# Optimization experiments

Measured on AMD Instinct MI355X. Metric: run time of the kernel, lower is better.

The kernel has to match this reference:

```python
import jax, jax.numpy as jnp
import numpy as np

EMB = 1024
FF = 1024
EPS = 1e-5

def _layernorm(x, g, b):
    mu = jnp.mean(x, axis=-1, keepdims=True)
    var = jnp.mean((x - mu) ** 2, axis=-1, keepdims=True)
    return (x - mu) * jax.lax.rsqrt(var + EPS) * g + b

def setup_inputs() -> dict:
    key = jax.random.key(0)
    ks = jax.random.split(key, 12)
    s = 1.0 / np.sqrt(EMB)
    x = jax.random.normal(ks[0], (4, 2048, EMB), dtype=jnp.float32)
    Wq = jax.random.normal(ks[1], (EMB, EMB), dtype=jnp.float32) * s
    bq = jnp.zeros((EMB,), jnp.float32)
    Wk = jax.random.normal(ks[2], (EMB, EMB), dtype=jnp.float32) * s
    bk = jnp.zeros((EMB,), jnp.float32)
    Wv = jax.random.normal(ks[3], (EMB, EMB), dtype=jnp.float32) * s
    bv = jnp.zeros((EMB,), jnp.float32)
    Wo = jax.random.normal(ks[4], (EMB, EMB), dtype=jnp.float32) * s
    bo = jnp.zeros((EMB,), jnp.float32)
    W1 = jax.random.normal(ks[5], (EMB, FF), dtype=jnp.float32) * s
    b1 = jnp.zeros((FF,), jnp.float32)
    W2 = jax.random.normal(ks[6], (FF, EMB), dtype=jnp.float32) * (1.0 / np.sqrt(FF))
    b2 = jnp.zeros((EMB,), jnp.float32)
    g1 = jnp.ones((EMB,), jnp.float32); be1 = jnp.zeros((EMB,), jnp.float32)
    g2 = jnp.ones((EMB,), jnp.float32); be2 = jnp.zeros((EMB,), jnp.float32)
    return {"x": x, "Wq": Wq, "bq": bq, "Wk": Wk, "bk": bk, "Wv": Wv, "bv": bv,
            "Wo": Wo, "bo": bo, "W1": W1, "b1": b1, "W2": W2, "b2": b2,
            "g1": g1, "be1": be1, "g2": g2, "be2": be2}

def reference(x, Wq, bq, Wk, bk, Wv, bv, Wo, bo, W1, b1, W2, b2, g1, be1, g2, be2):
    # pre-norm single-head self-attention + residual + FFN (dropout = identity, eval)
    xn = _layernorm(x, g1, be1)
    q = xn @ Wq + bq
    k = xn @ Wk + bk
    v = xn @ Wv + bv
    scores = jnp.einsum('bse,bte->bst', q, k) / jnp.sqrt(jnp.float32(EMB))
    w = jax.nn.softmax(scores, axis=-1)              # [B,S,S]
    attn = jnp.einsum('bst,bte->bse', w, v) @ Wo + bo
    x2 = x + attn
    xn2 = _layernorm(x2, g2, be2)
    ff = jax.nn.relu(xn2 @ W1 + b1) @ W2 + b2
    out = x2 + ff
    return (out, w)
```

## Files before the change

kernel.cpp:

```cpp
#include <hip/hip_runtime.h>

typedef __attribute__((ext_vector_type(8))) __bf16 bf16x8;
typedef __attribute__((ext_vector_type(4))) float f32x4;
typedef __attribute__((ext_vector_type(8))) ushort ushort8;

#define GLP(p) ((const __attribute__((address_space(1))) void*)(p))
#define LDP(p) ((__attribute__((address_space(3))) void*)(p))

__device__ __forceinline__ ushort f2b(float f) {
  union { float f; uint u; } c; c.f = f;
  uint u = c.u;
  uint r = (u + 0x7fffu + ((u >> 16) & 1u)) >> 16;
  return (ushort)r;
}

__device__ __forceinline__ void barrier_raw() {
  asm volatile("" ::: "memory");
  __builtin_amdgcn_s_barrier();
  asm volatile("" ::: "memory");
}
__device__ __forceinline__ void wait_lgkm0() {
  asm volatile("s_waitcnt lgkmcnt(0)" ::: "memory");
  __builtin_amdgcn_sched_barrier(0);
}

__device__ __forceinline__ float block_reduce_sum(float v, float* sm) {
#pragma unroll
  for (int off = 1; off < 64; off <<= 1) v += __shfl_xor(v, off);
  const int wave = threadIdx.x >> 6, lane = threadIdx.x & 63;
  __syncthreads();
  if (lane == 0) sm[wave] = v;
  __syncthreads();
  return sm[0] + sm[1] + sm[2] + sm[3];
}

__global__ __launch_bounds__(256) void wtrans6_kernel(
    const float* __restrict__ W0, const float* __restrict__ W1,
    const float* __restrict__ W2, const float* __restrict__ W3,
    const float* __restrict__ W4, const float* __restrict__ W5,
    ushort* __restrict__ T0, ushort* __restrict__ T1, ushort* __restrict__ T2,
    ushort* __restrict__ T3, ushort* __restrict__ T4, ushort* __restrict__ T5) {
  __shared__ float tile[32][33];
  const float* Ws[6] = {W0, W1, W2, W3, W4, W5};
  ushort* Ts[6] = {T0, T1, T2, T3, T4, T5};
  const float* W = Ws[blockIdx.z];
  ushort* Wt = Ts[blockIdx.z];
  const int K = 1024, N = 1024;
  const int n0 = blockIdx.x * 32, k0 = blockIdx.y * 32;
  const int tx = threadIdx.x, ty = threadIdx.y;
#pragma unroll
  for (int i = 0; i < 32; i += 8)
    tile[ty + i][tx] = W[(long)(k0 + ty + i) * N + n0 + tx];
  __syncthreads();
#pragma unroll
  for (int i = 0; i < 32; i += 8)
    Wt[(long)(n0 + ty + i) * K + k0 + tx] = f2b(tile[tx][ty + i]);
}

__global__ __launch_bounds__(256) void layernorm_kernel(
    const float* __restrict__ x, const float* __restrict__ g,
    const float* __restrict__ be, ushort* __restrict__ out) {
  __shared__ float sm[4];
  const long row = blockIdx.x;
  const float4 v = reinterpret_cast<const float4*>(x + row * 1024)[threadIdx.x];
  float s = v.x + v.y + v.z + v.w;
  s = block_reduce_sum(s, sm);
  const float mu = s * (1.0f / 1024.0f);
  const float dx = v.x - mu, dy = v.y - mu, dz = v.z - mu, dw = v.w - mu;
  float s2 = dx * dx + dy * dy + dz * dz + dw * dw;
  s2 = block_reduce_sum(s2, sm);
  const float rstd = rsqrtf(s2 * (1.0f / 1024.0f) + 1e-5f);
  const float4 gg = reinterpret_cast<const float4*>(g)[threadIdx.x];
  const float4 bb = reinterpret_cast<const float4*>(be)[threadIdx.x];
  ushort4 o;
  o.x = f2b(dx * rstd * gg.x + bb.x);
  o.y = f2b(dy * rstd * gg.y + bb.y);
  o.z = f2b(dz * rstd * gg.z + bb.z);
  o.w = f2b(dw * rstd * gg.w + bb.w);
  reinterpret_cast<ushort4*>(out + row * 1024)[threadIdx.x] = o;
}

__global__ __launch_bounds__(256) void softmax_kernel(
    float* __restrict__ s, ushort* __restrict__ wb) {
  __shared__ float sm[4];
  const long row = blockIdx.x;
  float4* r4 = reinterpret_cast<float4*>(s + row * 2048);
  float4 v0 = r4[threadIdx.x * 2];
  float4 v1 = r4[threadIdx.x * 2 + 1];
  float m = fmaxf(fmaxf(fmaxf(v0.x, v0.y), fmaxf(v0.z, v0.w)),
                  fmaxf(fmaxf(v1.x, v1.y), fmaxf(v1.z, v1.w)));
#pragma unroll
  for (int off = 1; off < 64; off <<= 1) m = fmaxf(m, __shfl_xor(m, off));
  const int wave = threadIdx.x >> 6, lane = threadIdx.x & 63;
  if (lane == 0) sm[wave] = m;
  __syncthreads();
  m = fmaxf(fmaxf(sm[0], sm[1]), fmaxf(sm[2], sm[3]));
  v0.x = expf(v0.x - m); v0.y = expf(v0.y - m);
  v0.z = expf(v0.z - m); v0.w = expf(v0.w - m);
  v1.x = expf(v1.x - m); v1.y = expf(v1.y - m);
  v1.z = expf(v1.z - m); v1.w = expf(v1.w - m);
  float sum = v0.x + v0.y + v0.z + v0.w + v1.x + v1.y + v1.z + v1.w;
  sum = block_reduce_sum(sum, sm);
  const float inv = 1.0f / sum;
  v0.x *= inv; v0.y *= inv; v0.z *= inv; v0.w *= inv;
  v1.x *= inv; v1.y *= inv; v1.z *= inv; v1.w *= inv;
  r4[threadIdx.x * 2] = v0;
  r4[threadIdx.x * 2 + 1] = v1;
  ushort8 o;
  o[0] = f2b(v0.x); o[1] = f2b(v0.y); o[2] = f2b(v0.z); o[3] = f2b(v0.w);
  o[4] = f2b(v1.x); o[5] = f2b(v1.y); o[6] = f2b(v1.z); o[7] = f2b(v1.w);
  *reinterpret_cast<ushort8*>(wb + row * 2048 + threadIdx.x * 8) = o;
}

#define EP_BF16 1
#define EP_F32 2
#define EP_BIAS 4
#define EP_RELU 8
#define EP_SCALE 16
#define EP_RESID 32
#define EP_TRANS 64

template <int FLAGS>
__global__ __launch_bounds__(256) void gemm_bt(
    const ushort* __restrict__ A, const ushort* __restrict__ Bt,
    float* __restrict__ Cf, ushort* __restrict__ Cb,
    const float* __restrict__ bias, const float* __restrict__ resid,
    int M, int N, int K, float scale, long sA, long sB, long sC) {
  A += (long)blockIdx.z * sA;
  Bt += (long)blockIdx.z * sB;
  const long coff = (long)blockIdx.z * sC;
  const int tileN = blockIdx.x * 128, tileM = blockIdx.y * 128;
  const int tid = threadIdx.x, lane = tid & 63, wave = tid >> 6;
  const int wm = tid >> 7, wn = (tid >> 6) & 1;
  __shared__ alignas(16) ushort As[2][128][32];
  __shared__ alignas(16) ushort Bs[2][128][32];
  f32x4 acc[4][4] = {};

  const int srow = wave * 32 + (lane >> 2);
  const int scol = (lane & 3) * 8;
  const ushort* aP0 = A + (long)(tileM + srow) * K + scol;
  const ushort* aP1 = aP0 + 16L * K;
  const ushort* bP0 = Bt + (long)(tileN + srow) * K + scol;
  const ushort* bP1 = bP0 + 16L * K;

#define STAGE(buf, kk)                                                                   \
  do {                                                                                   \
    __builtin_amdgcn_global_load_lds(GLP(aP0 + (kk)), LDP(&As[buf][wave * 32][0]), 16,   \
                                     0, 0);                                              \
    __builtin_amdgcn_global_load_lds(GLP(aP1 + (kk)), LDP(&As[buf][wave * 32 + 16][0]),  \
                                     16, 0, 0);                                          \
    __builtin_amdgcn_global_load_lds(GLP(bP0 + (kk)), LDP(&Bs[buf][wave * 32][0]), 16,   \
                                     0, 0);                                              \
    __builtin_amdgcn_global_load_lds(GLP(bP1 + (kk)), LDP(&Bs[buf][wave * 32 + 16][0]),  \
                                     16, 0, 0);                                          \
  } while (0)

  STAGE(0, 0);
  __syncthreads();
  int cur = 0;
  for (int kk = 0; kk < K; kk += 32) {
    const int nxt = cur ^ 1;
    if (kk + 32 < K) STAGE(nxt, kk + 32);
    bf16x8 a[4], b[4];
#pragma unroll
    for (int m = 0; m < 4; ++m)
      a[m] = *reinterpret_cast<const bf16x8*>(
          &As[cur][wm * 64 + m * 16 + (lane & 15)][(lane >> 4) * 8]);
#pragma unroll
    for (int n = 0; n < 4; ++n)
      b[n] = *reinterpret_cast<const bf16x8*>(
          &Bs[cur][wn * 64 + n * 16 + (lane & 15)][(lane >> 4) * 8]);
#pragma unroll
    for (int m = 0; m < 4; ++m)
#pragma unroll
      for (int n = 0; n < 4; ++n)
        acc[m][n] = __builtin_amdgcn_mfma_f32_16x16x32_bf16(a[m], b[n], acc[m][n], 0, 0, 0);
    __syncthreads();
    cur = nxt;
  }
#undef STAGE

  const int row0 = tileM + wm * 64 + ((lane >> 4) << 2);
  const int col0 = tileN + wn * 64 + (lane & 15);
#pragma unroll
  for (int n = 0; n < 4; ++n) {
    const int col = col0 + n * 16;
    const float bv = (FLAGS & EP_BIAS) ? bias[col] : 0.0f;
#pragma unroll
    for (int m = 0; m < 4; ++m) {
#pragma unroll
      for (int i = 0; i < 4; ++i) {
        const int row = row0 + m * 16 + i;
        float v = acc[m][n][i];
        if (FLAGS & EP_SCALE) v *= scale;
        v += bv;
        if (FLAGS & EP_RELU) v = fmaxf(v, 0.0f);
        if (FLAGS & EP_RESID) v += resid[coff + (long)row * N + col];
        if (FLAGS & EP_F32) Cf[coff + (long)row * N + col] = v;
        if (FLAGS & EP_BF16) {
          if (FLAGS & EP_TRANS)
            Cb[coff + (long)col * M + row] = f2b(v);
          else
            Cb[coff + (long)row * N + col] = f2b(v);
        }
      }
    }
  }
}

template <int MODE>
__global__ __launch_bounds__(512, 2) void gemm256(
    const ushort* __restrict__ A, const ushort* __restrict__ Bt,
    float* __restrict__ Cf,
    ushort* __restrict__ Cq, ushort* __restrict__ Ck, ushort* __restrict__ Cv,
    const float* __restrict__ b0, const float* __restrict__ b1,
    const float* __restrict__ b2,
    int M, int N, int K, float scale, long sA, long sB, long sC) {
  A += (long)blockIdx.z * sA;
  Bt += (long)blockIdx.z * sB;
  const long coff = (long)blockIdx.z * sC;
  const int tileN = blockIdx.x * 256, tileM = blockIdx.y * 256;
  const int tid = threadIdx.x, lane = tid & 63, wid = tid >> 6;
  const int wr = wid >> 2, wc = wid & 3;
  __shared__ ushort lds[4][2][8192];
  f32x4 acc[8][4] = {};

  const int NS = K >> 5;

  const ushort* aSrc = A + (long)(tileM + wid * 32 + (lane >> 2)) * K + (lane & 3) * 8;
  const ushort* bSrc = Bt + (long)(tileN + wid * 32 + (lane >> 2)) * K + (lane & 3) * 8;

#define STAGE_A256(s)                                                                    \
  do {                                                                                   \
    const int sl_ = (s) & 3;                                                             \
    __builtin_amdgcn_global_load_lds(GLP(aSrc + (long)(s) * 32),                         \
                                     LDP(&lds[sl_][0][(wid * 2 + 0) * 512]), 16, 0, 0);  \
    __builtin_amdgcn_global_load_lds(GLP(aSrc + 16L * K + (long)(s) * 32),               \
                                     LDP(&lds[sl_][0][(wid * 2 + 1) * 512]), 16, 0, 0);  \
  } while (0)
#define STAGE_B256(s)                                                                    \
  do {                                                                                   \
    const int sl_ = (s) & 3;                                                             \
    __builtin_amdgcn_global_load_lds(GLP(bSrc + (long)(s) * 32),                         \
                                     LDP(&lds[sl_][1][(wid * 2 + 0) * 512]), 16, 0, 0);  \
    __builtin_amdgcn_global_load_lds(GLP(bSrc + 16L * K + (long)(s) * 32),               \
                                     LDP(&lds[sl_][1][(wid * 2 + 1) * 512]), 16, 0, 0);  \
  } while (0)
#define LDA256(sl, f)                                                                    \
  (*reinterpret_cast<const bf16x8*>(                                                     \
      &lds[sl][0][(wr * 128 + (f) * 16 + (lane & 15)) * 32 + (lane >> 4) * 8]))
#define LDB256(sl, f)                                                                    \
  (*reinterpret_cast<const bf16x8*>(                                                     \
      &lds[sl][1][(wc * 64 + (f) * 16 + (lane & 15)) * 32 + (lane >> 4) * 8]))

  STAGE_A256(0); STAGE_B256(0);
  STAGE_A256(1); STAGE_B256(1);
  STAGE_A256(2); STAGE_B256(2);
  asm volatile("s_waitcnt vmcnt(8)" ::: "memory");
  barrier_raw();

  for (int s = 0; s < NS; ++s) {
    const int sl = s & 3;
    bf16x8 aF[4], bF[4];
#pragma unroll
    for (int f = 0; f < 4; ++f) aF[f] = LDA256(sl, f);
#pragma unroll
    for (int f = 0; f < 4; ++f) bF[f] = LDB256(sl, f);
    if (s + 3 < NS) STAGE_A256(s + 3);
    barrier_raw();
    wait_lgkm0();
    __builtin_amdgcn_s_setprio(1);
#pragma unroll
    for (int m = 0; m < 4; ++m)
#pragma unroll
      for (int n = 0; n < 4; ++n)
        acc[m][n] = __builtin_amdgcn_mfma_f32_16x16x32_bf16(aF[m], bF[n], acc[m][n], 0, 0, 0);
    __builtin_amdgcn_s_setprio(0);
    barrier_raw();
#pragma unroll
    for (int f = 0; f < 4; ++f) aF[f] = LDA256(sl, f + 4);
    if (s + 3 < NS) STAGE_B256(s + 3);
    barrier_raw();
    wait_lgkm0();
    __builtin_amdgcn_s_setprio(1);
#pragma unroll
    for (int m = 0; m < 4; ++m)
#pragma unroll
      for (int n = 0; n < 4; ++n)
        acc[m + 4][n] =
            __builtin_amdgcn_mfma_f32_16x16x32_bf16(aF[m], bF[n], acc[m + 4][n], 0, 0, 0);
    __builtin_amdgcn_s_setprio(0);
    if (s <= NS - 4) {
      asm volatile("s_waitcnt vmcnt(8)" ::: "memory");
    } else if (s == NS - 3) {
      asm volatile("s_waitcnt vmcnt(4)" ::: "memory");
    } else if (s == NS - 2) {
      asm volatile("s_waitcnt vmcnt(0)" ::: "memory");
    }
    barrier_raw();
  }
#undef STAGE_A256
#undef STAGE_B256
#undef LDA256
#undef LDB256

  const int r0 = tileM + wr * 128 + ((lane >> 4) << 2);
  const int c0 = tileN + wc * 64 + (lane & 15);
#pragma unroll
  for (int m = 0; m < 8; ++m) {
#pragma unroll
    for (int n = 0; n < 4; ++n) {
      const int col = c0 + n * 16;
#pragma unroll
      for (int i = 0; i < 4; ++i) {
        const int row = r0 + m * 16 + i;
        if (MODE == 0) {
          Cf[coff + (long)row * N + col] = acc[m][n][i] * scale;
        } else {
          const int seg = col >> 10, c = col & 1023;
          const float bias = (seg == 0) ? b0[c] : (seg == 1) ? b1[c] : b2[c];
          const float v = acc[m][n][i] + bias;
          if (seg == 0) {
            Cq[(long)row * 1024 + c] = f2b(v);
          } else if (seg == 1) {
            Ck[(long)row * 1024 + c] = f2b(v);
          } else {
            const long b = row >> 11;
            const int s0 = row & 2047;
            Cv[((b << 10) + c) * 2048 + s0] = f2b(v);
          }
        }
      }
    }
  }
}

extern "C" void kernel_launch(void* const* d_in, const int* in_sizes, int n_in,
                              void* d_out, int out_size, void* d_ws, size_t ws_size,
                              hipStream_t stream) {
  const int B = 4, S = 2048, E = 1024, FFD = 1024;
  const long MS = (long)B * S;
  const float* x   = (const float*)d_in[0];
  const float* Wq  = (const float*)d_in[1];
  const float* bq  = (const float*)d_in[2];
  const float* Wk  = (const float*)d_in[3];
  const float* bk  = (const float*)d_in[4];
  const float* Wv  = (const float*)d_in[5];
  const float* bv  = (const float*)d_in[6];
  const float* Wo  = (const float*)d_in[7];
  const float* bo  = (const float*)d_in[8];
  const float* W1  = (const float*)d_in[9];
  const float* b1  = (const float*)d_in[10];
  const float* W2  = (const float*)d_in[11];
  const float* b2  = (const float*)d_in[12];
  const float* g1  = (const float*)d_in[13];
  const float* be1 = (const float*)d_in[14];
  const float* g2  = (const float*)d_in[15];
  const float* be2 = (const float*)d_in[16];

  float* out  = (float*)d_out;
  float* wout = out + MS * E;

  ushort* xnA = (ushort*)d_ws;
  ushort* qB  = xnA + MS * E;
  ushort* kC  = qB + MS * E;
  ushort* vTD = kC + MS * E;
  ushort* wE  = vTD + MS * E;
  float*  x2F = (float*)(wE + (long)B * S * S);
  ushort* wts = (ushort*)(x2F + MS * E);
  ushort* WqT = wts;
  ushort* WkT = WqT + (long)E * E;
  ushort* WvT = WkT + (long)E * E;
  ushort* WoT = WvT + (long)E * E;
  ushort* W1T = WoT + (long)E * E;
  ushort* W2T = W1T + (long)E * FFD;

  hipLaunchKernelGGL(wtrans6_kernel, dim3(E / 32, E / 32, 6), dim3(32, 8), 0, stream,
                     Wq, Wk, Wv, Wo, W1, W2, WqT, WkT, WvT, WoT, W1T, W2T);

  hipLaunchKernelGGL(layernorm_kernel, dim3(MS), dim3(256), 0, stream, x, g1, be1, xnA);

  hipLaunchKernelGGL((gemm256<1>), dim3(3 * E / 256, MS / 256, 1), dim3(512), 0, stream,
                     xnA, WqT, (float*)nullptr, qB, kC, vTD, bq, bk, bv,
                     (int)MS, 3 * E, E, 1.0f, 0L, 0L, 0L);

  hipLaunchKernelGGL((gemm256<0>), dim3(S / 256, S / 256, B), dim3(512), 0, stream,
                     qB, kC, wout, (ushort*)nullptr, (ushort*)nullptr, (ushort*)nullptr,
                     (const float*)nullptr, (const float*)nullptr, (const float*)nullptr,
                     S, S, E, 0.03125f, (long)S * E, (long)S * E, (long)S * S);

  hipLaunchKernelGGL(softmax_kernel, dim3(B * S), dim3(256), 0, stream, wout, wE);

  hipLaunchKernelGGL((gemm_bt<EP_BF16>), dim3(E / 128, S / 128, B), dim3(256), 0, stream,
                     wE, vTD, (float*)nullptr, qB, (const float*)nullptr,
                     (const float*)nullptr, S, E, S, 1.0f, (long)S * S, (long)E * S,
                     (long)S * E);

  hipLaunchKernelGGL((gemm_bt<EP_F32 | EP_BIAS | EP_RESID>), dim3(E / 128, MS / 128, 1),
                     dim3(256), 0, stream, qB, WoT, x2F, (ushort*)nullptr, bo, x,
                     (int)MS, E, E, 1.0f, 0L, 0L, 0L);

  hipLaunchKernelGGL(layernorm_kernel, dim3(MS), dim3(256), 0, stream, x2F, g2, be2, xnA);

  hipLaunchKernelGGL((gemm_bt<EP_BF16 | EP_BIAS | EP_RELU>), dim3(FFD / 128, MS / 128, 1),
                     dim3(256), 0, stream, xnA, W1T, (float*)nullptr, kC, b1,
                     (const float*)nullptr, (int)MS, FFD, E, 1.0f, 0L, 0L, 0L);

  hipLaunchKernelGGL((gemm_bt<EP_F32 | EP_BIAS | EP_RESID>), dim3(E / 128, MS / 128, 1),
                     dim3(256), 0, stream, kC, W2T, out, (ushort*)nullptr, b2, x2F,
                     (int)MS, E, FFD, 1.0f, 0L, 0L, 0L);
}
```

Baseline: 364.3 us.

## Restructure 256x256 GEMM mainloop into 8-wave ping-pong with swizzled 64-wide K tiles

The gemm256 main loop now uses K tiles of 64 instead of 32, with two double-buffered LDS stages split into A/B halves. Loads are spread across four MFMA quadrant phases per tile, so global-to-LDS staging is interleaved with compute at finer granularity. An XOR swizzle on the LDS column index is meant to avoid bank conflicts on the wider rows. This adds barriers and manual vmcnt/lgkmcnt bookkeeping, so a wrong count could cause races. It also assumes K is a multiple of 128.

```diff
diff --git a/kernel.cpp b/kernel.cpp
--- a/kernel.cpp
+++ b/kernel.cpp
@@ -222,87 +222,116 @@
   const int tileN = blockIdx.x * 256, tileM = blockIdx.y * 256;
   const int tid = threadIdx.x, lane = tid & 63, wid = tid >> 6;
   const int wr = wid >> 2, wc = wid & 3;
-  __shared__ ushort lds[4][2][8192];
+  __shared__ alignas(16) ushort AB[2][2][2][8192];
   f32x4 acc[8][4] = {};
-
-  const int NS = K >> 5;
-
-  const ushort* aSrc = A + (long)(tileM + wid * 32 + (lane >> 2)) * K + (lane & 3) * 8;
-  const ushort* bSrc = Bt + (long)(tileN + wid * 32 + (lane >> 2)) * K + (lane & 3) * 8;
-
-#define STAGE_A256(s)                                                                    \
+  const int NT = K >> 6;
+  const int NI = NT >> 1;
+
+  const int srw = lane >> 3;
+  const int scl = ((lane & 7) ^ srw) * 8;
+  const ushort* aBase = A + (long)(tileM + wid * 16 + srw) * K + scl;
+  const ushort* bBase = Bt + (long)(tileN + wid * 16 + srw) * K + scl;
+
+#define STG_A(buf, half, T)                                                              \
   do {                                                                                   \
-    const int sl_ = (s) & 3;                                                             \
-    __builtin_amdgcn_global_load_lds(GLP(aSrc + (long)(s) * 32),                         \
-                                     LDP(&lds[sl_][0][(wid * 2 + 0) * 512]), 16, 0, 0);  \
-    __builtin_amdgcn_global_load_lds(GLP(aSrc + 16L * K + (long)(s) * 32),               \
-                                     LDP(&lds[sl_][0][(wid * 2 + 1) * 512]), 16, 0, 0);  \
+    __builtin_amdgcn_global_load_lds(GLP(aBase + (long)(half) * 128 * K + (long)(T) * 64), \
+                                     LDP(&AB[0][buf][half][(wid * 2 + 0) * 512]), 16, 0, 0); \
+    __builtin_amdgcn_global_load_lds(                                                    \
+        GLP(aBase + (long)(half) * 128 * K + 8L * K + (long)(T) * 64),                   \
+        LDP(&AB[0][buf][half][(wid * 2 + 1) * 512]), 16, 0, 0);                          \
   } while (0)
-#define STAGE_B256(s)                                                                    \
+#define STG_B(buf, half, T)                                                              \
   do {                                                                                   \
-    const int sl_ = (s) & 3;                                                             \
-    __builtin_amdgcn_global_load_lds(GLP(bSrc + (long)(s) * 32),                         \
-                                     LDP(&lds[sl_][1][(wid * 2 + 0) * 512]), 16, 0, 0);  \
-    __builtin_amdgcn_global_load_lds(GLP(bSrc + 16L * K + (long)(s) * 32),               \
-                                     LDP(&lds[sl_][1][(wid * 2 + 1) * 512]), 16, 0, 0);  \
+    __builtin_amdgcn_global_load_lds(GLP(bBase + (long)(half) * 128 * K + (long)(T) * 64), \
+                                     LDP(&AB[1][buf][half][(wid * 2 + 0) * 512]), 16, 0, 0); \
+    __builtin_amdgcn_global_load_lds(                                                    \
+        GLP(bBase + (long)(half) * 128 * K + 8L * K + (long)(T) * 64),                   \
+        LDP(&AB[1][buf][half][(wid * 2 + 1) * 512]), 16, 0, 0);                          \
   } while (0)
-#define LDA256(sl, f)                                                                    \
+#define LDA(buf, m, kk)                                                                  \
   (*reinterpret_cast<const bf16x8*>(                                                     \
-      &lds[sl][0][(wr * 128 + (f) * 16 + (lane & 15)) * 32 + (lane >> 4) * 8]))
-#define LDB256(sl, f)                                                                    \
+      &AB[0][buf][wr][((m) * 16 + (lane & 15)) * 64 +                                    \
+                      ((((kk) * 4 + (lane >> 4)) ^ (lane & 7)) * 8)]))
+#define LDB(buf, n, kk)                                                                  \
   (*reinterpret_cast<const bf16x8*>(                                                     \
-      &lds[sl][1][(wc * 64 + (f) * 16 + (lane & 15)) * 32 + (lane >> 4) * 8]))
-
-  STAGE_A256(0); STAGE_B256(0);
-  STAGE_A256(1); STAGE_B256(1);
-  STAGE_A256(2); STAGE_B256(2);
-  asm volatile("s_waitcnt vmcnt(8)" ::: "memory");
+      &AB[1][buf][wc >> 1][((wc & 1) * 64 + (n) * 16 + (lane & 15)) * 64 +               \
+                           ((((kk) * 4 + (lane >> 4)) ^ (lane & 7)) * 8)]))
+#define MFQ(ml, nl, av)                                                                  \
+  do {                                                                                   \
+    _Pragma("unroll") for (int m_ = 0; m_ < 4; ++m_) {                                   \
+      _Pragma("unroll") for (int n_ = 0; n_ < 2; ++n_) {                                 \
+        acc[(ml) + m_][(nl) + n_] = __builtin_amdgcn_mfma_f32_16x16x32_bf16(             \
+            av[m_][0], b[(nl) + n_][0], acc[(ml) + m_][(nl) + n_], 0, 0, 0);             \
+        acc[(ml) + m_][(nl) + n_] = __builtin_amdgcn_mfma_f32_16x16x32_bf16(             \
+            av[m_][1], b[(nl) + n_][1], acc[(ml) + m_][(nl) + n_], 0, 0, 0);             \
+      }                                                                                  \
+    }                                                                                    \
+  } while (0)
+
+  STG_B(0, 0, 0); STG_B(0, 1, 0); STG_A(0, 0, 0); STG_A(0, 1, 0);
+  STG_B(1, 0, 1); STG_A(1, 0, 1); STG_A(1, 1, 1);
+  asm volatile("s_waitcnt vmcnt(6)" ::: "memory");
   barrier_raw();
 
-  for (int s = 0; s < NS; ++s) {
-    const int sl = s & 3;
-    bf16x8 aF[4], bF[4];
-#pragma unroll
-    for (int f = 0; f < 4; ++f) aF[f] = LDA256(sl, f);
-#pragma unroll
-    for (int f = 0; f < 4; ++f) bF[f] = LDB256(sl, f);
-    if (s + 3 < NS) STAGE_A256(s + 3);
-    barrier_raw();
-    wait_lgkm0();
-    __builtin_amdgcn_s_setprio(1);
-#pragma unroll
-    for (int m = 0; m < 4; ++m)
-#pragma unroll
-      for (int n = 0; n < 4; ++n)
-        acc[m][n] = __builtin_amdgcn_mfma_f32_16x16x32_bf16(aF[m], bF[n], acc[m][n], 0, 0, 0);
-    __builtin_amdgcn_s_setprio(0);
-    barrier_raw();
-#pragma unroll
-    for (int f = 0; f < 4; ++f) aF[f] = LDA256(sl, f + 4);
-    if (s + 3 < NS) STAGE_B256(s + 3);
-    barrier_raw();
-    wait_lgkm0();
-    __builtin_amdgcn_s_setprio(1);
-#pragma unroll
-    for (int m = 0; m < 4; ++m)
-#pragma unroll
-      for (int n = 0; n < 4; ++n)
-        acc[m + 4][n] =
-            __builtin_amdgcn_mfma_f32_16x16x32_bf16(aF[m], bF[n], acc[m + 4][n], 0, 0, 0);
-    __builtin_amdgcn_s_setprio(0);
-    if (s <= NS - 4) {
-      asm volatile("s_waitcnt vmcnt(8)" ::: "memory");
-    } else if (s == NS - 3) {
-      asm volatile("s_waitcnt vmcnt(4)" ::: "memory");
-    } else if (s == NS - 2) {
-      asm volatile("s_waitcnt vmcnt(0)" ::: "memory");
-    }
+  for (int i = 0; i < NI; ++i) {
+    const bool last = (i == NI - 1);
+    const int T1 = 2 * i + 1, T2 = 2 * i + 2, T3 = 2 * i + 3;
+    bf16x8 a[4][2], a2[4][2], b[4][2];
+#pragma unroll
+    for (int n = 0; n < 4; ++n) { b[n][0] = LDB(0, n, 0); b[n][1] = LDB(0, n, 1); }
+#pragma unroll
+    for (int m = 0; m < 4; ++m) { a[m][0] = LDA(0, m, 0); a[m][1] = LDA(0, m, 1); }
+    STG_B(1, 1, T1);
+    asm volatile("s_waitcnt lgkmcnt(8)" ::: "memory");
+    barrier_raw(); wait_lgkm0();
+    __builtin_amdgcn_s_setprio(1); MFQ(0, 0, a); __builtin_amdgcn_s_setprio(0);
+    barrier_raw();
+#pragma unroll
+    for (int m = 0; m < 4; ++m) { a2[m][0] = LDA(0, m + 4, 0); a2[m][1] = LDA(0, m + 4, 1); }
+    if (!last) STG_B(0, 0, T2);
+    barrier_raw(); wait_lgkm0();
+    __builtin_amdgcn_s_setprio(1); MFQ(0, 2, a); __builtin_amdgcn_s_setprio(0);
+    barrier_raw();
+    if (!last) STG_B(0, 1, T2);
+    barrier_raw(); wait_lgkm0();
+    __builtin_amdgcn_s_setprio(1); MFQ(4, 2, a2); __builtin_amdgcn_s_setprio(0);
+    barrier_raw();
+    if (!last) STG_A(0, 0, T2);
+    barrier_raw(); wait_lgkm0();
+    __builtin_amdgcn_s_setprio(1); MFQ(4, 0, a2); __builtin_amdgcn_s_setprio(0);
+    if (!last) { asm volatile("s_waitcnt vmcnt(6)" ::: "memory"); }
+    else       { asm volatile("s_waitcnt vmcnt(0)" ::: "memory"); }
+    barrier_raw();
+#pragma unroll
+    for (int n = 0; n < 4; ++n) { b[n][0] = LDB(1, n, 0); b[n][1] = LDB(1, n, 1); }
+#pragma unroll
+    for (int m = 0; m < 4; ++m) { a[m][0] = LDA(1, m, 0); a[m][1] = LDA(1, m, 1); }
+    if (!last) STG_A(0, 1, T2);
+    asm volatile("s_waitcnt lgkmcnt(8)" ::: "memory");
+    barrier_raw(); wait_lgkm0();
+    __builtin_amdgcn_s_setprio(1); MFQ(0, 0, a); __builtin_amdgcn_s_setprio(0);
+    barrier_raw();
+#pragma unroll
+    for (int m = 0; m < 4; ++m) { a2[m][0] = LDA(1, m + 4, 0); a2[m][1] = LDA(1, m + 4, 1); }
+    if (!last) STG_B(1, 0, T3);
+    barrier_raw(); wait_lgkm0();
+    __builtin_amdgcn_s_setprio(1); MFQ(0, 2, a); __builtin_amdgcn_s_setprio(0);
+    barrier_raw();
+    if (!last) STG_A(1, 0, T3);
+    barrier_raw(); wait_lgkm0();
+    __builtin_amdgcn_s_setprio(1); MFQ(4, 2, a2); __builtin_amdgcn_s_setprio(0);
+    barrier_raw();
+    if (!last) STG_A(1, 1, T3);
+    barrier_raw(); wait_lgkm0();
+    __builtin_amdgcn_s_setprio(1); MFQ(4, 0, a2); __builtin_amdgcn_s_setprio(0);
+    if (!last) { asm volatile("s_waitcnt vmcnt(6)" ::: "memory"); }
     barrier_raw();
   }
-#undef STAGE_A256
-#undef STAGE_B256
-#undef LDA256
-#undef LDB256
+#undef STG_A
+#undef STG_B
+#undef LDA
+#undef LDB
+#undef MFQ
 
   const int r0 = tileM + wr * 128 + ((lane >> 4) << 2);
   const int c0 = tileN + wc * 64 + (lane & 15);
@@ -325,9 +354,9 @@
           } else if (seg == 1) {
             Ck[(long)row * 1024 + c] = f2b(v);
           } else {
-            const long b = row >> 11;
+            const long bb = row >> 11;
             const int s0 = row & 2047;
-            Cv[((b << 10) + c) * 2048 + s0] = f2b(v);
+            Cv[((bb << 10) + c) * 2048 + s0] = f2b(v);
           }
         }
       }
```

Measured after the change: 359.4 us. No clear change (-1.3%).
